# Kernel optimization log

Hardware: AMD Instinct MI355X
Metric: run time of the kernel (lower is better)

The kernel has to match this reference:

```python
import jax, jax.numpy as jnp
import numpy as np

D_MODEL = 1024
N_HEADS = 16
D_HEAD = D_MODEL // N_HEADS
B = 2
Q_LEN = 1024
MEM_LEN = 1024
K_LEN = MEM_LEN + Q_LEN


def _split_heads(x, n_heads):
    b, t, d = x.shape
    return x.reshape(b, t, n_heads, d // n_heads).transpose(0, 2, 1, 3)


def _rel_shift(x):
    # x: [b, h, q, k] -> Transformer-XL relative shift
    b, h, q_len, k_len = x.shape
    x = jnp.pad(x, ((0, 0), (0, 0), (0, 0), (1, 0)))
    x = x.reshape(b, h, k_len + 1, q_len)
    x = x[:, :, 1:, :]
    return x.reshape(b, h, q_len, k_len)


def setup_inputs() -> dict:
    key = jax.random.key(0)
    ks = jax.random.split(key, 10)
    s = 1.0 / np.sqrt(D_MODEL)  # lecun_normal-ish scale for kernels
    return {
        "h": jax.random.normal(ks[0], (B, Q_LEN, D_MODEL), jnp.float32),
        "mem": jax.random.normal(ks[1], (B, MEM_LEN, D_MODEL), jnp.float32),
        "r": jax.random.normal(ks[2], (K_LEN, D_MODEL), jnp.float32),
        "Wq": jax.random.normal(ks[3], (D_MODEL, D_MODEL), jnp.float32) * s,
        "Wk": jax.random.normal(ks[4], (D_MODEL, D_MODEL), jnp.float32) * s,
        "Wv": jax.random.normal(ks[5], (D_MODEL, D_MODEL), jnp.float32) * s,
        "Wr": jax.random.normal(ks[6], (D_MODEL, D_MODEL), jnp.float32) * s,
        "Wo": jax.random.normal(ks[7], (D_MODEL, D_MODEL), jnp.float32) * s,
        "r_w_bias": jnp.zeros((N_HEADS, D_HEAD), jnp.float32),
        "r_r_bias": jnp.zeros((N_HEADS, D_HEAD), jnp.float32),
    }


def reference(h, mem, r, Wq, Wk, Wv, Wr, Wo, r_w_bias, r_r_bias):
    k_len = mem.shape[1] + h.shape[1]
    cat = jnp.concatenate([mem, h], axis=1)           # [b, k, d]
    q = _split_heads(h @ Wq, N_HEADS)                  # [b, h, q, dh]
    k = _split_heads(cat @ Wk, N_HEADS)                # [b, h, k, dh]
    v = _split_heads(cat @ Wv, N_HEADS)                # [b, h, k, dh]
    r_head = (r @ Wr).reshape(k_len, N_HEADS, D_HEAD).transpose(1, 0, 2)  # [h, k, dh]

    qw = q + r_w_bias[None, :, None, :]
    ac = jnp.einsum('bhqd,bhkd->bhqk', qw, k)          # content score
    qr = q + r_r_bias[None, :, None, :]
    bd = _rel_shift(jnp.einsum('bhqd,hkd->bhqk', qr, r_head))  # position score

    attn_score = (ac + bd) / jnp.sqrt(jnp.array(D_HEAD, jnp.float32))
    attn_prob = jax.nn.softmax(attn_score, axis=-1)
    attn_vec = jnp.einsum('bhqk,bhkd->bhqd', attn_prob, v)
    b, nh, t, dh = attn_vec.shape
    attn_vec = attn_vec.transpose(0, 2, 1, 3).reshape(b, t, nh * dh)
    return attn_vec @ Wo
```

## Files before the change

kernel.cpp:

```cpp
#include <hip/hip_runtime.h>

#define DM 1024
#define NH 16
#define DH 64
#define QL 1024
#define KL 2048

typedef short s16x8 __attribute__((ext_vector_type(8)));
typedef float f32x4 __attribute__((ext_vector_type(4)));

__device__ __forceinline__ unsigned short f2bf(float f) {
  unsigned int u = __builtin_bit_cast(unsigned int, f);
  u += 0x7fffu + ((u >> 16) & 1u);
  return (unsigned short)(u >> 16);
}
__device__ __forceinline__ float bf2f(unsigned short b) {
  unsigned int u = ((unsigned int)b) << 16;
  return __builtin_bit_cast(float, u);
}
__device__ __forceinline__ f32x4 mfma16(s16x8 a, s16x8 b, f32x4 c) {
  return __builtin_amdgcn_mfma_f32_16x16x32_bf16(a, b, c, 0, 0, 0);
}
__device__ __forceinline__ void gl2lds16(const void* g, void* l) {
  __builtin_amdgcn_global_load_lds(
      (const __attribute__((address_space(1))) unsigned int*)g,
      (__attribute__((address_space(3))) unsigned int*)l, 16, 0, 0);
}


__global__ __launch_bounds__(256) void prep_all(
    const float* __restrict__ h, const float* __restrict__ mem, const float* __restrict__ r,
    const float* __restrict__ Wq, const float* __restrict__ Wk, const float* __restrict__ Wv,
    const float* __restrict__ Wr, const float* __restrict__ Wo,
    unsigned short* __restrict__ catb, unsigned short* __restrict__ rb,
    unsigned short* __restrict__ wqt, unsigned short* __restrict__ wkvt,
    unsigned short* __restrict__ wrt,
    unsigned short* __restrict__ wohi, unsigned short* __restrict__ wolo)
{
  __shared__ unsigned short tH[64][72];
  __shared__ unsigned short tL[64][72];
  if (blockIdx.x < 6144) {
    int idx = blockIdx.x * 256 + threadIdx.x;
    if (idx < 1048576) {
      int e = idx * 4;
      int row = e >> 10, col = e & 1023;
      int b = row >> 11, t = row & 2047;
      const float* s = (t < 1024) ? &mem[((size_t)(b * 1024 + t)) * 1024 + col]
                                  : &h[((size_t)(b * 1024 + t - 1024)) * 1024 + col];
      float4 v = *(const float4*)s;
      *(ushort4*)&catb[e] = make_ushort4(f2bf(v.x), f2bf(v.y), f2bf(v.z), f2bf(v.w));
    } else {
      int e = (idx - 1048576) * 4;
      float4 v = *(const float4*)&r[e];
      *(ushort4*)&rb[e] = make_ushort4(f2bf(v.x), f2bf(v.y), f2bf(v.z), f2bf(v.w));
    }
    return;
  }
  int q = blockIdx.x - 6144;
  int job = q >> 8;
  int tb = q & 255;
  int sr0 = (tb >> 4) * 64, sc0 = (tb & 15) * 64;
  const float* src = (job == 0) ? Wq : (job == 1) ? Wk : (job == 2) ? Wv : (job == 3) ? Wr : Wo;
  int tid = threadIdx.x;
  int rr = tid >> 4, c4 = (tid & 15) * 4;
#pragma unroll
  for (int i = 0; i < 4; ++i) {
    int row = rr + i * 16;
    float4 v = *(const float4*)&src[(size_t)(sr0 + row) * 1024 + sc0 + c4];
    float vv[4] = {v.x, v.y, v.z, v.w};
#pragma unroll
    for (int j = 0; j < 4; ++j) {
      unsigned short hi = f2bf(vv[j]);
      tH[c4 + j][row] = hi;
      if (job == 4) tL[c4 + j][row] = f2bf(vv[j] - bf2f(hi));
    }
  }
  __syncthreads();
  unsigned short* dst = (job == 0) ? wqt : (job == 1) ? wkvt
                      : (job == 2) ? (wkvt + (size_t)1024 * 1024)
                      : (job == 3) ? wrt : wohi;
#pragma unroll
  for (int i = 0; i < 4; ++i) {
    int row = rr + i * 16;
    size_t o = (size_t)(sc0 + row) * 1024 + sr0 + c4;
    *(ushort4*)&dst[o] = make_ushort4(tH[row][c4], tH[row][c4 + 1], tH[row][c4 + 2], tH[row][c4 + 3]);
    if (job == 4)
      *(ushort4*)&wolo[o] = make_ushort4(tL[row][c4], tL[row][c4 + 1], tL[row][c4 + 2], tL[row][c4 + 3]);
  }
}

__global__ __launch_bounds__(256) void gemm_all(
    const unsigned short* __restrict__ catb, const unsigned short* __restrict__ rb,
    const unsigned short* __restrict__ wqt, const unsigned short* __restrict__ wkvt,
    const unsigned short* __restrict__ wrt,
    const float* __restrict__ rwb, const float* __restrict__ rrb,
    unsigned short* __restrict__ qwP, unsigned short* __restrict__ qrP,
    unsigned short* __restrict__ kP, unsigned short* __restrict__ vP,
    unsigned short* __restrict__ rP)
{
  __shared__ __align__(16) unsigned short As[128 * 32];
  __shared__ __align__(16) unsigned short Bs[128 * 32];
  int blk = blockIdx.x, tid = threadIdx.x;
  int job, mb, nb;
  const unsigned short *A, *Bt;
  if (blk < 128)      { job = 0; A = catb; Bt = wqt;  mb = blk >> 3; nb = blk & 7; }
  else if (blk < 640) { job = 1; A = catb; Bt = wkvt; int q = blk - 128; mb = q >> 4; nb = q & 15; }
  else                { job = 2; A = rb;   Bt = wrt;  int q = blk - 640; mb = q >> 3; nb = q & 7; }

  const int w = tid >> 6;
  const int r0 = tid >> 2;
  const int c0u = (tid & 3) * 8;
  int ga_r0 = mb * 128 + r0, ga_r1 = mb * 128 + 64 + r0;
  if (job == 0) {
    ga_r0 = ((ga_r0 >> 10) << 11) + 1024 + (ga_r0 & 1023);
    ga_r1 = ((ga_r1 >> 10) << 11) + 1024 + (ga_r1 & 1023);
  }
  const unsigned short* gA0 = A + (size_t)ga_r0 * 1024 + c0u;
  const unsigned short* gA1 = A + (size_t)ga_r1 * 1024 + c0u;
  const unsigned short* gB0 = Bt + (size_t)(nb * 128 + r0) * 1024 + c0u;
  const unsigned short* gB1 = Bt + (size_t)(nb * 128 + 64 + r0) * 1024 + c0u;
  char* lA0 = (char*)As + w * 1024;  char* lA1 = (char*)As + 4096 + w * 1024;
  char* lB0 = (char*)Bs + w * 1024;  char* lB1 = (char*)Bs + 4096 + w * 1024;

  const int lane = tid & 63;
  const int lc = lane & 15, quad = lane >> 4;
  const int wm = (w & 1) * 64, wn = (w >> 1) * 64;

  f32x4 acc[4][4];
#pragma unroll
  for (int mt = 0; mt < 4; ++mt)
#pragma unroll
    for (int nt = 0; nt < 4; ++nt) { acc[mt][nt][0] = 0.f; acc[mt][nt][1] = 0.f; acc[mt][nt][2] = 0.f; acc[mt][nt][3] = 0.f; }

  for (int k0 = 0; k0 < 1024; k0 += 32) {
    __syncthreads();
    gl2lds16(gA0 + k0, lA0);
    gl2lds16(gA1 + k0, lA1);
    gl2lds16(gB0 + k0, lB0);
    gl2lds16(gB1 + k0, lB1);
    __syncthreads();
    s16x8 af[4], bf[4];
#pragma unroll
    for (int mt = 0; mt < 4; ++mt) af[mt] = *(const s16x8*)&As[(wm + mt * 16 + lc) * 32 + quad * 8];
#pragma unroll
    for (int nt = 0; nt < 4; ++nt) bf[nt] = *(const s16x8*)&Bs[(wn + nt * 16 + lc) * 32 + quad * 8];
#pragma unroll
    for (int mt = 0; mt < 4; ++mt)
#pragma unroll
      for (int nt = 0; nt < 4; ++nt) acc[mt][nt] = mfma16(af[mt], bf[nt], acc[mt][nt]);
  }

#pragma unroll
  for (int mt = 0; mt < 4; ++mt) {
    int t4 = mb * 128 + wm + mt * 16 + quad * 4;
#pragma unroll
    for (int nt = 0; nt < 4; ++nt) {
      int n = nb * 128 + wn + nt * 16 + lc;
      if (job == 0) {
        int hh = n >> 6, dh = n & 63;
        int f = dh >> 5, qd = (dh >> 3) & 3, j = dh & 7;
        float bw = rwb[n], br = rrb[n];
        int bb = t4 >> 10, trow = t4 & 1023;
        size_t tbb = ((((size_t)(bb * NH + hh) * 64 + (trow >> 4)) * 2 + f) * 512) + qd * 128 + j;
        int l0 = trow & 15;
#pragma unroll
        for (int rr = 0; rr < 4; ++rr) {
          qwP[tbb + (l0 + rr) * 8] = f2bf(acc[mt][nt][rr] + bw);
          qrP[tbb + (l0 + rr) * 8] = f2bf(acc[mt][nt][rr] + br);
        }
      } else if (job == 1) {
        int bb = t4 >> 11, t = t4 & 2047;
        if (n < 1024) {
          int hh = n >> 6, dh = n & 63;
          int f = dh >> 5, qd = (dh >> 3) & 3, j = dh & 7;
          size_t tbb = ((((size_t)(bb * NH + hh) * 128 + (t >> 4)) * 2 + f) * 512) + qd * 128 + j;
          int l0 = t & 15;
#pragma unroll
          for (int rr = 0; rr < 4; ++rr)
            kP[tbb + (l0 + rr) * 8] = f2bf(acc[mt][nt][rr]);
        } else {
          int n2 = n - 1024, hh = n2 >> 6, dh = n2 & 63;
          int bhv = bb * NH + hh;
          int kt = t >> 5;
          int ntv = dh >> 4;
          int lanev = (((t >> 3) & 3) << 4) + (dh & 15);
          ushort4 pk = make_ushort4(f2bf(acc[mt][nt][0]), f2bf(acc[mt][nt][1]),
                                    f2bf(acc[mt][nt][2]), f2bf(acc[mt][nt][3]));
          *(ushort4*)&vP[(((size_t)bhv * 64 + kt) * 4 + ntv) * 512 + lanev * 8 + (t & 7)] = pk;
        }
      } else {
        int hh = n >> 6, dh = n & 63;
        int f = dh >> 5, qd = (dh >> 3) & 3, j = dh & 7;
        size_t tbb = (((size_t)hh * 128 + (t4 >> 4)) * 2 + f) * 512 + qd * 128 + j;
        int l0 = t4 & 15;
#pragma unroll
        for (int rr = 0; rr < 4; ++rr)
          rP[tbb + (l0 + rr) * 8] = f2bf(acc[mt][nt][rr]);
      }
    }
  }
}

#define BDSTR 2058
__global__ __launch_bounds__(512, 4) void attn(
    const unsigned short* __restrict__ qwP, const unsigned short* __restrict__ qrP,
    const unsigned short* __restrict__ kP, const unsigned short* __restrict__ vP,
    const unsigned short* __restrict__ rP,
    unsigned short* __restrict__ avhi, unsigned short* __restrict__ avlo)
{
  __shared__ __align__(16) unsigned short bdS[17 * BDSTR];
  __shared__ __align__(16) unsigned short pS[8 * 16 * 36];
  float* oS = (float*)bdS;
  float* lS = (float*)bdS + 8192;

  const int tid = threadIdx.x;
  const int w = tid >> 6, lane = tid & 63;
  const int lc = lane & 15, quad = lane >> 4;
  const int is = blockIdx.x & 63, h = (blockIdx.x >> 6) & 15, b = blockIdx.x >> 10;
  const int i0 = is * 16;
  const size_t bh = (size_t)b * NH + h;

  const unsigned short* qwP_p = qwP + bh * 65536;
  const unsigned short* qrP_p = qrP + bh * 65536;
  const unsigned short* kP_p  = kP + bh * 131072;
  const unsigned short* vP_p  = vP + bh * (size_t)KL * DH + lane * 8;
  const unsigned short* rP_p  = rP + (size_t)h * 131072;

  {
    s16x8 qa00 = *(const s16x8*)(qrP_p + is * 1024 + lane * 8);
    s16x8 qa01 = *(const s16x8*)(qrP_p + is * 1024 + 512 + lane * 8);
    int r1 = i0 + 16 + lc; if (r1 > 1023) r1 = 1023;
    int off1 = (r1 >> 4) * 1024 + (quad * 16 + (r1 & 15)) * 8;
    s16x8 qa10 = *(const s16x8*)(qrP_p + off1);
    s16x8 qa11 = *(const s16x8*)(qrP_p + off1 + 512);
    const int xt0 = w * 16;
    const unsigned short* rp = rP_p + xt0 * 1024 + lane * 8;
    s16x8 rf0 = *(const s16x8*)rp;
    s16x8 rf1 = *(const s16x8*)(rp + 512);
    for (int xt = xt0; xt < xt0 + 16; ++xt) {
      s16x8 cf0 = rf0, cf1 = rf1;
      if (xt + 1 < xt0 + 16) {
        const unsigned short* rpn = rP_p + (xt + 1) * 1024 + lane * 8;
        rf0 = *(const s16x8*)rpn;
        rf1 = *(const s16x8*)(rpn + 512);
      }
      f32x4 c0; c0[0] = 0.f; c0[1] = 0.f; c0[2] = 0.f; c0[3] = 0.f;
      f32x4 c1 = c0;
      c0 = mfma16(qa00, cf0, c0); c0 = mfma16(qa01, cf1, c0);
      c1 = mfma16(qa10, cf0, c1); c1 = mfma16(qa11, cf1, c1);
      int col = xt * 16 + lc;
#pragma unroll
      for (int rr = 0; rr < 4; ++rr) bdS[(quad * 4 + rr) * BDSTR + col] = f2bf(c0[rr]);
      if (lane < 16) bdS[16 * BDSTR + col] = f2bf(c1[0]);
    }
  }
  __syncthreads();

  s16x8 qwf0 = *(const s16x8*)(qwP_p + is * 1024 + lane * 8);
  s16x8 qwf1 = *(const s16x8*)(qwP_p + is * 1024 + 512 + lane * 8);

  f32x4 O[4];
#pragma unroll
  for (int nt = 0; nt < 4; ++nt) { O[nt][0] = 0.f; O[nt][1] = 0.f; O[nt][2] = 0.f; O[nt][3] = 0.f; }
  float lsum[4] = {0.f, 0.f, 0.f, 0.f};
  unsigned short* pw = pS + w * 16 * 36;
  int ebase[4];
#pragma unroll
  for (int rr = 0; rr < 4; ++rr) ebase[rr] = lc - (quad * 4 + rr) - i0;

  auto score = [&](int k0, float p[2][4]) {
    float bd[2][4];
#pragma unroll
    for (int tt = 0; tt < 2; ++tt)
#pragma unroll
      for (int rr = 0; rr < 4; ++rr) {
        int row = quad * 4 + rr;
        int d = k0 + tt * 16 + ebase[rr];
        int am = row * BDSTR + (d + 1023);
        int aw = (row + 1) * BDSTR + (d - 1026);
        unsigned short vb = bdS[(d <= 1024) ? am : aw];
        bd[tt][rr] = (d == 1025) ? 0.0f : bf2f(vb);
      }
#pragma unroll
    for (int tt = 0; tt < 2; ++tt) {
      const unsigned short* kp = kP_p + (size_t)((k0 >> 4) + tt) * 1024 + lane * 8;
      s16x8 kf0 = *(const s16x8*)kp;
      s16x8 kf1 = *(const s16x8*)(kp + 512);
      f32x4 c; c[0] = 0.f; c[1] = 0.f; c[2] = 0.f; c[3] = 0.f;
      c = mfma16(qwf0, kf0, c);
      c = mfma16(qwf1, kf1, c);
#pragma unroll
      for (int rr = 0; rr < 4; ++rr) {
        p[tt][rr] = __expf(fmaf(c[rr] + bd[tt][rr], 0.125f, -12.0f));
        lsum[rr] += p[tt][rr];
      }
    }
  };
  auto storeP = [&](float p[2][4]) {
#pragma unroll
    for (int rr = 0; rr < 4; ++rr) {
      int row = quad * 4 + rr;
      pw[row * 36 + lc]      = f2bf(p[0][rr]);
      pw[row * 36 + 16 + lc] = f2bf(p[1][rr]);
    }
  };
  auto loadV = [&](int k0, s16x8 vf[4]) {
    const unsigned short* base = vP_p + (size_t)(k0 >> 5) * 2048;
#pragma unroll
    for (int nt = 0; nt < 4; ++nt)
      vf[nt] = *(const s16x8*)(base + nt * 512);
  };

  s16x8 vfPrev[4];
  {
    float p[2][4];
    score(w * 256, p);
    storeP(p);
    loadV(w * 256, vfPrev);
  }
#pragma unroll 1
  for (int it = 1; it < 8; ++it) {
    const int k0 = w * 256 + it * 32;
    float p[2][4];
    score(k0, p);
    __builtin_amdgcn_s_waitcnt(0xC07F);
    s16x8 pf = *(const s16x8*)(pw + lc * 36 + quad * 8);
#pragma unroll
    for (int nt = 0; nt < 4; ++nt) O[nt] = mfma16(pf, vfPrev[nt], O[nt]);
    loadV(k0, vfPrev);
    storeP(p);
  }
  {
    __builtin_amdgcn_s_waitcnt(0xC07F);
    s16x8 pf = *(const s16x8*)(pw + lc * 36 + quad * 8);
#pragma unroll
    for (int nt = 0; nt < 4; ++nt) O[nt] = mfma16(pf, vfPrev[nt], O[nt]);
  }

#pragma unroll
  for (int msk = 1; msk <= 8; msk <<= 1)
#pragma unroll
    for (int rr = 0; rr < 4; ++rr) lsum[rr] += __shfl_xor(lsum[rr], msk);

  __syncthreads();
#pragma unroll
  for (int nt = 0; nt < 4; ++nt)
#pragma unroll
    for (int rr = 0; rr < 4; ++rr)
      oS[(w * 16 + quad * 4 + rr) * 64 + nt * 16 + lc] = O[nt][rr];
  if (lc == 0) {
#pragma unroll
    for (int rr = 0; rr < 4; ++rr) lS[w * 16 + quad * 4 + rr] = lsum[rr];
  }
  __syncthreads();

  if (tid < 256) {
    int r = tid >> 4, c0 = (tid & 15) * 4;
    float L = 0.f, a0 = 0.f, a1 = 0.f, a2 = 0.f, a3 = 0.f;
#pragma unroll
    for (int wv = 0; wv < 8; ++wv) {
      L += lS[wv * 16 + r];
      const float* op = oS + (wv * 16 + r) * 64 + c0;
      a0 += op[0]; a1 += op[1]; a2 += op[2]; a3 += op[3];
    }
    float inv = 1.0f / L;
    float v[4] = {a0 * inv, a1 * inv, a2 * inv, a3 * inv};
    unsigned short hi[4], lo[4];
#pragma unroll
    for (int j = 0; j < 4; ++j) {
      hi[j] = f2bf(v[j]);
      lo[j] = f2bf(v[j] - bf2f(hi[j]));
    }
    size_t oidx = ((size_t)(b * QL + i0 + r)) * DM + h * DH + c0;
    *(ushort4*)&avhi[oidx] = make_ushort4(hi[0], hi[1], hi[2], hi[3]);
    *(ushort4*)&avlo[oidx] = make_ushort4(lo[0], lo[1], lo[2], lo[3]);
  }
}

__global__ __launch_bounds__(256) void gemm_final(
    const unsigned short* __restrict__ avhi, const unsigned short* __restrict__ avlo,
    const unsigned short* __restrict__ wohi, const unsigned short* __restrict__ wolo,
    float* __restrict__ out)
{
  __shared__ __align__(16) unsigned short S[4][64 * 32];
  int blk = blockIdx.x, tid = threadIdx.x;
  int mb = blk >> 4, nb = blk & 15;

  const int w = tid >> 6, lane = tid & 63;
  const int srow = w * 16 + (lane >> 2);
  const int scu = (lane & 3) * 8;
  const size_t arow = (size_t)(mb * 64 + srow) * 1024 + scu;
  const size_t brow = (size_t)(nb * 64 + srow) * 1024 + scu;
  char* l0 = (char*)S[0] + w * 1024;
  char* l1 = (char*)S[1] + w * 1024;
  char* l2 = (char*)S[2] + w * 1024;
  char* l3 = (char*)S[3] + w * 1024;

  const int lc = lane & 15, quad = lane >> 4;
  const int wm = (w & 1) * 32, wn = (w >> 1) * 32;

  f32x4 acc[2][2];
#pragma unroll
  for (int mt = 0; mt < 2; ++mt)
#pragma unroll
    for (int nt = 0; nt < 2; ++nt) { acc[mt][nt][0] = 0.f; acc[mt][nt][1] = 0.f; acc[mt][nt][2] = 0.f; acc[mt][nt][3] = 0.f; }

  for (int k0 = 0; k0 < 1024; k0 += 32) {
    __syncthreads();
    gl2lds16(avhi + arow + k0, l0);
    gl2lds16(avlo + arow + k0, l1);
    gl2lds16(wohi + brow + k0, l2);
    gl2lds16(wolo + brow + k0, l3);
    __syncthreads();
    s16x8 ah[2], al[2], bh[2], bl[2];
#pragma unroll
    for (int mt = 0; mt < 2; ++mt) {
      int off = (wm + mt * 16 + lc) * 32 + quad * 8;
      ah[mt] = *(const s16x8*)&S[0][off];
      al[mt] = *(const s16x8*)&S[1][off];
    }
#pragma unroll
    for (int nt = 0; nt < 2; ++nt) {
      int off = (wn + nt * 16 + lc) * 32 + quad * 8;
      bh[nt] = *(const s16x8*)&S[2][off];
      bl[nt] = *(const s16x8*)&S[3][off];
    }
#pragma unroll
    for (int mt = 0; mt < 2; ++mt)
#pragma unroll
      for (int nt = 0; nt < 2; ++nt) {
        acc[mt][nt] = mfma16(ah[mt], bh[nt], acc[mt][nt]);
        acc[mt][nt] = mfma16(ah[mt], bl[nt], acc[mt][nt]);
        acc[mt][nt] = mfma16(al[mt], bh[nt], acc[mt][nt]);
      }
  }

#pragma unroll
  for (int mt = 0; mt < 2; ++mt)
#pragma unroll
    for (int nt = 0; nt < 2; ++nt) {
      int n = nb * 64 + wn + nt * 16 + lc;
#pragma unroll
      for (int rr = 0; rr < 4; ++rr) {
        int m = mb * 64 + wm + mt * 16 + quad * 4 + rr;
        out[(size_t)m * 1024 + n] = acc[mt][nt][rr];
      }
    }
}

extern "C" void kernel_launch(void* const* d_in, const int* in_sizes, int n_in,
                              void* d_out, int out_size, void* d_ws, size_t ws_size,
                              hipStream_t stream) {
  (void)in_sizes; (void)n_in; (void)out_size; (void)ws_size;
  const float* h   = (const float*)d_in[0];
  const float* mem = (const float*)d_in[1];
  const float* r   = (const float*)d_in[2];
  const float* Wq  = (const float*)d_in[3];
  const float* Wk  = (const float*)d_in[4];
  const float* Wv  = (const float*)d_in[5];
  const float* Wr  = (const float*)d_in[6];
  const float* Wo  = (const float*)d_in[7];
  const float* rwb = (const float*)d_in[8];
  const float* rrb = (const float*)d_in[9];
  float* out = (float*)d_out;

  char* ws = (char*)d_ws;
  unsigned short* catb = (unsigned short*)(ws + 0);
  unsigned short* rb   = (unsigned short*)(ws + 8388608);
  unsigned short* wqt  = (unsigned short*)(ws + 12582912);
  unsigned short* wkvt = (unsigned short*)(ws + 14680064);
  unsigned short* wrt  = (unsigned short*)(ws + 18874368);
  unsigned short* wohi = (unsigned short*)(ws + 20971520);
  unsigned short* wolo = (unsigned short*)(ws + 23068672);
  unsigned short* qwP  = (unsigned short*)(ws + 25165824);
  unsigned short* qrP  = (unsigned short*)(ws + 29360128);
  unsigned short* kPb  = (unsigned short*)(ws + 33554432);
  unsigned short* vPb  = (unsigned short*)(ws + 41943040);
  unsigned short* rPb  = (unsigned short*)(ws + 50331648);
  unsigned short* avhi = (unsigned short*)(ws + 54525952);
  unsigned short* avlo = (unsigned short*)(ws + 58720256);

  prep_all<<<7424, 256, 0, stream>>>(h, mem, r, Wq, Wk, Wv, Wr, Wo,
                                     catb, rb, wqt, wkvt, wrt, wohi, wolo);
  gemm_all<<<768, 256, 0, stream>>>(catb, rb, wqt, wkvt, wrt, rwb, rrb,
                                    qwP, qrP, kPb, vPb, rPb);
  attn<<<2048, 512, 0, stream>>>(qwP, qrP, kPb, vPb, rPb, avhi, avlo);
  gemm_final<<<512, 256, 0, stream>>>(avhi, avlo, wohi, wolo, out);
}
```

Before: 250.1 us.

## Deepen GEMM K-steps, prefetch K in attention, skip unused bd MFMAs, use exp2

Both projection GEMMs now stage 64-wide K slices per barrier pair instead of 32, which halves the number of syncthreads round trips at the cost of twice the shared memory. The attention kernel prefetches the next K fragments one iteration ahead and seeds the QK MFMA accumulator with the bd term. It also switches to exp2 with pre-folded constants. The extra row of the positional-score tile is computed only for columns the rel-shift can actually read, removing redundant MFMAs. Together these target barrier overhead, load latency and wasted matrix work, while adding register pressure.

```diff
diff --git a/kernel.cpp b/kernel.cpp
--- a/kernel.cpp
+++ b/kernel.cpp
@@ -98,8 +98,8 @@
     unsigned short* __restrict__ kP, unsigned short* __restrict__ vP,
     unsigned short* __restrict__ rP)
 {
-  __shared__ __align__(16) unsigned short As[128 * 32];
-  __shared__ __align__(16) unsigned short Bs[128 * 32];
+  __shared__ __align__(16) unsigned short As[2 * 128 * 32];
+  __shared__ __align__(16) unsigned short Bs[2 * 128 * 32];
   int blk = blockIdx.x, tid = threadIdx.x;
   int job, mb, nb;
   const unsigned short *A, *Bt;
@@ -132,22 +132,29 @@
 #pragma unroll
     for (int nt = 0; nt < 4; ++nt) { acc[mt][nt][0] = 0.f; acc[mt][nt][1] = 0.f; acc[mt][nt][2] = 0.f; acc[mt][nt][3] = 0.f; }
 
-  for (int k0 = 0; k0 < 1024; k0 += 32) {
+  for (int k0 = 0; k0 < 1024; k0 += 64) {
     __syncthreads();
     gl2lds16(gA0 + k0, lA0);
     gl2lds16(gA1 + k0, lA1);
     gl2lds16(gB0 + k0, lB0);
     gl2lds16(gB1 + k0, lB1);
+    gl2lds16(gA0 + k0 + 32, lA0 + 8192);
+    gl2lds16(gA1 + k0 + 32, lA1 + 8192);
+    gl2lds16(gB0 + k0 + 32, lB0 + 8192);
+    gl2lds16(gB1 + k0 + 32, lB1 + 8192);
     __syncthreads();
-    s16x8 af[4], bf[4];
-#pragma unroll
-    for (int mt = 0; mt < 4; ++mt) af[mt] = *(const s16x8*)&As[(wm + mt * 16 + lc) * 32 + quad * 8];
-#pragma unroll
-    for (int nt = 0; nt < 4; ++nt) bf[nt] = *(const s16x8*)&Bs[(wn + nt * 16 + lc) * 32 + quad * 8];
-#pragma unroll
-    for (int mt = 0; mt < 4; ++mt)
-#pragma unroll
-      for (int nt = 0; nt < 4; ++nt) acc[mt][nt] = mfma16(af[mt], bf[nt], acc[mt][nt]);
+#pragma unroll
+    for (int s = 0; s < 2; ++s) {
+      s16x8 af[4], bfr[4];
+#pragma unroll
+      for (int mt = 0; mt < 4; ++mt) af[mt] = *(const s16x8*)&As[s * 4096 + (wm + mt * 16 + lc) * 32 + quad * 8];
+#pragma unroll
+      for (int nt = 0; nt < 4; ++nt) bfr[nt] = *(const s16x8*)&Bs[s * 4096 + (wn + nt * 16 + lc) * 32 + quad * 8];
+#pragma unroll
+      for (int mt = 0; mt < 4; ++mt)
+#pragma unroll
+        for (int nt = 0; nt < 4; ++nt) acc[mt][nt] = mfma16(af[mt], bfr[nt], acc[mt][nt]);
+    }
   }
 
 #pragma unroll
@@ -227,6 +234,7 @@
   const unsigned short* rP_p  = rP + (size_t)h * 131072;
 
   {
+    const int cmax = 1006 - i0;
     s16x8 qa00 = *(const s16x8*)(qrP_p + is * 1024 + lane * 8);
     s16x8 qa01 = *(const s16x8*)(qrP_p + is * 1024 + 512 + lane * 8);
     int r1 = i0 + 16 + lc; if (r1 > 1023) r1 = 1023;
@@ -245,13 +253,15 @@
         rf1 = *(const s16x8*)(rpn + 512);
       }
       f32x4 c0; c0[0] = 0.f; c0[1] = 0.f; c0[2] = 0.f; c0[3] = 0.f;
-      f32x4 c1 = c0;
       c0 = mfma16(qa00, cf0, c0); c0 = mfma16(qa01, cf1, c0);
-      c1 = mfma16(qa10, cf0, c1); c1 = mfma16(qa11, cf1, c1);
       int col = xt * 16 + lc;
 #pragma unroll
       for (int rr = 0; rr < 4; ++rr) bdS[(quad * 4 + rr) * BDSTR + col] = f2bf(c0[rr]);
-      if (lane < 16) bdS[16 * BDSTR + col] = f2bf(c1[0]);
+      if (xt * 16 <= cmax) {
+        f32x4 c1; c1[0] = 0.f; c1[1] = 0.f; c1[2] = 0.f; c1[3] = 0.f;
+        c1 = mfma16(qa10, cf0, c1); c1 = mfma16(qa11, cf1, c1);
+        if (lane < 16) bdS[16 * BDSTR + col] = f2bf(c1[0]);
+      }
     }
   }
   __syncthreads();
@@ -268,8 +278,7 @@
 #pragma unroll
   for (int rr = 0; rr < 4; ++rr) ebase[rr] = lc - (quad * 4 + rr) - i0;
 
-  auto score = [&](int k0, float p[2][4]) {
-    float bd[2][4];
+  auto gatherBD = [&](int k0, float bd[2][4]) {
 #pragma unroll
     for (int tt = 0; tt < 2; ++tt)
 #pragma unroll
@@ -281,19 +290,35 @@
         unsigned short vb = bdS[(d <= 1024) ? am : aw];
         bd[tt][rr] = (d == 1025) ? 0.0f : bf2f(vb);
       }
-#pragma unroll
-    for (int tt = 0; tt < 2; ++tt) {
-      const unsigned short* kp = kP_p + (size_t)((k0 >> 4) + tt) * 1024 + lane * 8;
-      s16x8 kf0 = *(const s16x8*)kp;
-      s16x8 kf1 = *(const s16x8*)(kp + 512);
-      f32x4 c; c[0] = 0.f; c[1] = 0.f; c[2] = 0.f; c[3] = 0.f;
-      c = mfma16(qwf0, kf0, c);
-      c = mfma16(qwf1, kf1, c);
-#pragma unroll
-      for (int rr = 0; rr < 4; ++rr) {
-        p[tt][rr] = __expf(fmaf(c[rr] + bd[tt][rr], 0.125f, -12.0f));
-        lsum[rr] += p[tt][rr];
-      }
+  };
+  auto loadK4 = [&](int k0, s16x8& a0, s16x8& a1, s16x8& b0, s16x8& b1) {
+    const unsigned short* kp = kP_p + (size_t)(k0 >> 4) * 1024 + lane * 8;
+    a0 = *(const s16x8*)kp;
+    a1 = *(const s16x8*)(kp + 512);
+    b0 = *(const s16x8*)(kp + 1024);
+    b1 = *(const s16x8*)(kp + 1536);
+  };
+  const float E2S = 0.18033688011112042f;
+  const float E2B = -17.312340490667562f;
+  auto qkExp = [&](const s16x8& a0, const s16x8& a1, const s16x8& b0, const s16x8& b1,
+                   const float bd[2][4], float p[2][4]) {
+    f32x4 c;
+    c[0] = bd[0][0]; c[1] = bd[0][1]; c[2] = bd[0][2]; c[3] = bd[0][3];
+    c = mfma16(qwf0, a0, c);
+    c = mfma16(qwf1, a1, c);
+#pragma unroll
+    for (int rr = 0; rr < 4; ++rr) {
+      p[0][rr] = __builtin_amdgcn_exp2f(fmaf(c[rr], E2S, E2B));
+      lsum[rr] += p[0][rr];
+    }
+    f32x4 d;
+    d[0] = bd[1][0]; d[1] = bd[1][1]; d[2] = bd[1][2]; d[3] = bd[1][3];
+    d = mfma16(qwf0, b0, d);
+    d = mfma16(qwf1, b1, d);
+#pragma unroll
+    for (int rr = 0; rr < 4; ++rr) {
+      p[1][rr] = __builtin_amdgcn_exp2f(fmaf(d[rr], E2S, E2B));
+      lsum[rr] += p[1][rr];
     }
   };
   auto storeP = [&](float p[2][4]) {
@@ -311,24 +336,35 @@
       vf[nt] = *(const s16x8*)(base + nt * 512);
   };
 
+  s16x8 ka0, ka1, kb0, kb1;
   s16x8 vfPrev[4];
+  loadK4(w * 256, ka0, ka1, kb0, kb1);
+  loadV(w * 256, vfPrev);
   {
-    float p[2][4];
-    score(w * 256, p);
+    float bd[2][4], p[2][4];
+    gatherBD(w * 256, bd);
+    s16x8 na0, na1, nb0, nb1;
+    loadK4(w * 256 + 32, na0, na1, nb0, nb1);
+    qkExp(ka0, ka1, kb0, kb1, bd, p);
     storeP(p);
-    loadV(w * 256, vfPrev);
+    ka0 = na0; ka1 = na1; kb0 = nb0; kb1 = nb1;
   }
 #pragma unroll 1
   for (int it = 1; it < 8; ++it) {
     const int k0 = w * 256 + it * 32;
-    float p[2][4];
-    score(k0, p);
     __builtin_amdgcn_s_waitcnt(0xC07F);
     s16x8 pf = *(const s16x8*)(pw + lc * 36 + quad * 8);
+    float bd[2][4], p[2][4];
+    gatherBD(k0, bd);
+    s16x8 na0, na1, nb0, nb1;
+    const int kn = k0 + ((it < 7) ? 32 : 0);
+    loadK4(kn, na0, na1, nb0, nb1);
 #pragma unroll
     for (int nt = 0; nt < 4; ++nt) O[nt] = mfma16(pf, vfPrev[nt], O[nt]);
     loadV(k0, vfPrev);
+    qkExp(ka0, ka1, kb0, kb1, bd, p);
     storeP(p);
+    ka0 = na0; ka1 = na1; kb0 = nb0; kb1 = nb1;
   }
   {
     __builtin_amdgcn_s_waitcnt(0xC07F);
@@ -382,7 +418,7 @@
     const unsigned short* __restrict__ wohi, const unsigned short* __restrict__ wolo,
     float* __restrict__ out)
 {
-  __shared__ __align__(16) unsigned short S[4][64 * 32];
+  __shared__ __align__(16) unsigned short S[4][2][64 * 32];
   int blk = blockIdx.x, tid = threadIdx.x;
   int mb = blk >> 4, nb = blk & 15;
 
@@ -391,10 +427,10 @@
   const int scu = (lane & 3) * 8;
   const size_t arow = (size_t)(mb * 64 + srow) * 1024 + scu;
   const size_t brow = (size_t)(nb * 64 + srow) * 1024 + scu;
-  char* l0 = (char*)S[0] + w * 1024;
-  char* l1 = (char*)S[1] + w * 1024;
-  char* l2 = (char*)S[2] + w * 1024;
-  char* l3 = (char*)S[3] + w * 1024;
+  char* l0 = (char*)&S[0][0][0] + w * 1024;
+  char* l1 = (char*)&S[1][0][0] + w * 1024;
+  char* l2 = (char*)&S[2][0][0] + w * 1024;
+  char* l3 = (char*)&S[3][0][0] + w * 1024;
 
   const int lc = lane & 15, quad = lane >> 4;
   const int wm = (w & 1) * 32, wn = (w >> 1) * 32;
@@ -405,34 +441,41 @@
 #pragma unroll
     for (int nt = 0; nt < 2; ++nt) { acc[mt][nt][0] = 0.f; acc[mt][nt][1] = 0.f; acc[mt][nt][2] = 0.f; acc[mt][nt][3] = 0.f; }
 
-  for (int k0 = 0; k0 < 1024; k0 += 32) {
+  for (int k0 = 0; k0 < 1024; k0 += 64) {
     __syncthreads();
     gl2lds16(avhi + arow + k0, l0);
+    gl2lds16(avhi + arow + k0 + 32, l0 + 4096);
     gl2lds16(avlo + arow + k0, l1);
+    gl2lds16(avlo + arow + k0 + 32, l1 + 4096);
     gl2lds16(wohi + brow + k0, l2);
+    gl2lds16(wohi + brow + k0 + 32, l2 + 4096);
     gl2lds16(wolo + brow + k0, l3);
+    gl2lds16(wolo + brow + k0 + 32, l3 + 4096);
     __syncthreads();
-    s16x8 ah[2], al[2], bh[2], bl[2];
-#pragma unroll
-    for (int mt = 0; mt < 2; ++mt) {
-      int off = (wm + mt * 16 + lc) * 32 + quad * 8;
-      ah[mt] = *(const s16x8*)&S[0][off];
-      al[mt] = *(const s16x8*)&S[1][off];
-    }
-#pragma unroll
-    for (int nt = 0; nt < 2; ++nt) {
-      int off = (wn + nt * 16 + lc) * 32 + quad * 8;
-      bh[nt] = *(const s16x8*)&S[2][off];
-      bl[nt] = *(const s16x8*)&S[3][off];
-    }
-#pragma unroll
-    for (int mt = 0; mt < 2; ++mt)
+#pragma unroll
+    for (int s = 0; s < 2; ++s) {
+      s16x8 ah[2], al[2], bh[2], bl[2];
+#pragma unroll
+      for (int mt = 0; mt < 2; ++mt) {
+        int off = (wm + mt * 16 + lc) * 32 + quad * 8;
+        ah[mt] = *(const s16x8*)&S[0][s][off];
+        al[mt] = *(const s16x8*)&S[1][s][off];
+      }
 #pragma unroll
       for (int nt = 0; nt < 2; ++nt) {
-        acc[mt][nt] = mfma16(ah[mt], bh[nt], acc[mt][nt]);
-        acc[mt][nt] = mfma16(ah[mt], bl[nt], acc[mt][nt]);
-        acc[mt][nt] = mfma16(al[mt], bh[nt], acc[mt][nt]);
-      }
+        int off = (wn + nt * 16 + lc) * 32 + quad * 8;
+        bh[nt] = *(const s16x8*)&S[2][s][off];
+        bl[nt] = *(const s16x8*)&S[3][s][off];
+      }
+#pragma unroll
+      for (int mt = 0; mt < 2; ++mt)
+#pragma unroll
+        for (int nt = 0; nt < 2; ++nt) {
+          acc[mt][nt] = mfma16(ah[mt], bh[nt], acc[mt][nt]);
+          acc[mt][nt] = mfma16(ah[mt], bl[nt], acc[mt][nt]);
+          acc[mt][nt] = mfma16(al[mt], bh[nt], acc[mt][nt]);
+        }
+    }
   }
 
 #pragma unroll
```

After: 260.3 us. +4.1%, slower.
